# Kernel optimization log

Hardware: AMD Instinct MI355X
Metric: run time of the kernel (lower is better)

Reference implementation:

```python
import jax, jax.numpy as jnp
import numpy as np

N, E = 50000, 800000
IN_DIM, HIDDEN, HEADS, EDGE_DIM, OUT_DIM = 128, 64, 4, 16, 1
NEG_SLOPE = 0.2


def gat_conv(x, src, dst, edge_attr, W, We, att_src, att_dst, att_edge, bias, heads, out_ch, concat):
    n = x.shape[0]
    h = (x @ W).reshape(n, heads, out_ch)                     # [N,H,C]
    a_src = jnp.einsum('nhc,hc->nh', h, att_src)              # [N,H]
    a_dst = jnp.einsum('nhc,hc->nh', h, att_dst)
    e = (edge_attr @ We).reshape(-1, heads, out_ch)           # [E,H,C]
    a_e = jnp.einsum('ehc,hc->eh', e, att_edge)               # [E,H]
    alpha = jax.nn.leaky_relu(a_src[src] + a_dst[dst] + a_e, NEG_SLOPE)  # [E,H]
    # per-destination-node softmax
    amax = jax.ops.segment_max(alpha, dst, num_segments=n)
    ex = jnp.exp(alpha - amax[dst])
    denom = jax.ops.segment_sum(ex, dst, num_segments=n)
    alpha = ex / (denom[dst] + 1e-16)
    msg = h[src] * alpha[..., None]                           # [E,H,C]
    out = jax.ops.segment_sum(msg, dst, num_segments=n)       # [N,H,C]
    out = out.reshape(n, heads * out_ch) if concat else out.mean(axis=1)
    return out + bias


def setup_inputs() -> dict:
    key = jax.random.key(0)
    ks = jax.random.split(key, 16)
    s = 0.1
    inp = {
        'x': jax.random.normal(ks[0], (N, IN_DIM), jnp.float32),
        'edge_index': jax.random.randint(ks[1], (2, E), 0, N, jnp.int32),
        'edge_attr': jax.random.normal(ks[2], (E, EDGE_DIM), jnp.float32),
        # layer 1: heads=4, concat=True
        'W1': jax.random.normal(ks[3], (IN_DIM, HEADS * HIDDEN), jnp.float32) * s,
        'We1': jax.random.normal(ks[4], (EDGE_DIM, HEADS * HIDDEN), jnp.float32) * s,
        'as1': jax.random.normal(ks[5], (HEADS, HIDDEN), jnp.float32) * s,
        'ad1': jax.random.normal(ks[6], (HEADS, HIDDEN), jnp.float32) * s,
        'ae1': jax.random.normal(ks[7], (HEADS, HIDDEN), jnp.float32) * s,
        'b1': jnp.zeros((HEADS * HIDDEN,), jnp.float32),
        # layer 2: heads=1, concat=False
        'W2': jax.random.normal(ks[8], (HEADS * HIDDEN, HIDDEN), jnp.float32) * s,
        'We2': jax.random.normal(ks[9], (EDGE_DIM, HIDDEN), jnp.float32) * s,
        'as2': jax.random.normal(ks[10], (1, HIDDEN), jnp.float32) * s,
        'ad2': jax.random.normal(ks[11], (1, HIDDEN), jnp.float32) * s,
        'ae2': jax.random.normal(ks[12], (1, HIDDEN), jnp.float32) * s,
        'b2': jnp.zeros((HIDDEN,), jnp.float32),
        'Wlin': jax.random.normal(ks[13], (HIDDEN, OUT_DIM), jnp.float32) * s,
        'blin': jnp.zeros((OUT_DIM,), jnp.float32),
    }
    return inp


def reference(x, edge_index, edge_attr, W1, We1, as1, ad1, ae1, b1, W2, We2, as2, ad2, ae2, b2, Wlin, blin):
    src, dst = edge_index[0], edge_index[1]
    h = jax.nn.relu(gat_conv(x, src, dst, edge_attr, W1, We1, as1, ad1, ae1, b1, HEADS, HIDDEN, True))
    h = jax.nn.relu(gat_conv(h, src, dst, edge_attr, W2, We2, as2, ad2, ae2, b2, 1, HIDDEN, False))
    return h @ Wlin + blin
```

## Files before the change

### kernel.cpp

```cpp
#include <hip/hip_runtime.h>
#include <math.h>

#define IN_DIM 128
#define HID 64
#define HEADS 4
#define EDGE_DIM 16
#define L1_OUT 256
#define NEG_SLOPE 0.2f
#define PAD 64

typedef __attribute__((ext_vector_type(8))) _Float16 half8_t;
typedef __attribute__((ext_vector_type(4))) _Float16 half4_t;
typedef __attribute__((ext_vector_type(4))) float floatx4;

__global__ __launch_bounds__(256) void prep_kernel(
    const float* __restrict__ W1, const float* __restrict__ as1, const float* __restrict__ ad1,
    const float* __restrict__ W2, const float* __restrict__ as2, const float* __restrict__ ad2,
    const float* __restrict__ We1, const float* __restrict__ ae1,
    const float* __restrict__ We2, const float* __restrict__ ae2,
    _Float16* __restrict__ W1t, _Float16* __restrict__ W2t,
    float* __restrict__ q1, float* __restrict__ q2) {
    int id = blockIdx.x * 256 + threadIdx.x;
    if (id < 272 * 128) {
        int n = id >> 7, k = id & 127;
        float v = 0.f;
        if (n < 256) v = W1[k * 256 + n];
        else if (n < 260) { int h = n - 256; float s = 0.f;
            for (int c = 0; c < 64; ++c) s += W1[k * 256 + h * 64 + c] * as1[h * 64 + c]; v = s; }
        else if (n < 264) { int h = n - 260; float s = 0.f;
            for (int c = 0; c < 64; ++c) s += W1[k * 256 + h * 64 + c] * ad1[h * 64 + c]; v = s; }
        W1t[id] = (_Float16)v;
        return;
    }
    id -= 272 * 128;
    if (id < 80 * 256) {
        int n = id >> 8, k = id & 255;
        float v = 0.f;
        if (n < 64) v = W2[k * 64 + n];
        else if (n == 64) { float s = 0.f; for (int c = 0; c < 64; ++c) s += W2[k * 64 + c] * as2[c]; v = s; }
        else if (n == 65) { float s = 0.f; for (int c = 0; c < 64; ++c) s += W2[k * 64 + c] * ad2[c]; v = s; }
        W2t[id] = (_Float16)v;
        return;
    }
    id -= 80 * 256;
    if (id < 64) {
        int k = id >> 2, h = id & 3;
        float s = 0.f;
        for (int c = 0; c < 64; ++c) s += We1[k * 256 + h * 64 + c] * ae1[h * 64 + c];
        q1[id] = s;
        return;
    }
    id -= 64;
    if (id < 16) {
        float s = 0.f;
        for (int c = 0; c < 64; ++c) s += We2[id * 64 + c] * ae2[c];
        q2[id] = s;
    }
}

__global__ __launch_bounds__(256) void scatter_edge_kernel(
    const int* __restrict__ src, const int* __restrict__ dst,
    const float* __restrict__ ea, const float* __restrict__ q1,
    const float* __restrict__ q2, int* __restrict__ deg,
    float4* __restrict__ rec, int E) {
    __shared__ float q[80];
    if (threadIdx.x < 64) q[threadIdx.x] = q1[threadIdx.x];
    else if (threadIdx.x < 80) q[threadIdx.x] = q2[threadIdx.x - 64];
    __syncthreads();
    int e = blockIdx.x * 256 + threadIdx.x;
    if (e >= E) return;
    const float4* p = (const float4*)(ea + (size_t)e * EDGE_DIM);
    float4 v0 = p[0], v1 = p[1], v2 = p[2], v3 = p[3];
    int sn = src[e];
    int d = dst[e];
    float a[16] = {v0.x, v0.y, v0.z, v0.w, v1.x, v1.y, v1.z, v1.w,
                   v2.x, v2.y, v2.z, v2.w, v3.x, v3.y, v3.z, v3.w};
    float4 r1;
    float* rp = (float*)&r1;
#pragma unroll
    for (int h = 0; h < 4; ++h) {
        float s = 0.f;
#pragma unroll
        for (int k = 0; k < 16; ++k) s += a[k] * q[k * 4 + h];
        rp[h] = s;
    }
    float r2 = 0.f;
#pragma unroll
    for (int k = 0; k < 16; ++k) r2 += a[k] * q[64 + k];
    int rank = atomicAdd(&deg[d], 1);
    if (rank >= PAD) return;
    size_t pos = (size_t)d * PAD + rank;
    float4 lo;
    lo.x = __int_as_float(sn); lo.y = r2; lo.z = 0.f; lo.w = 0.f;
    rec[pos * 2] = lo;
    rec[pos * 2 + 1] = r1;
}

template <int NTOT, int NFEAT, int HATT, bool A32>
__global__ __launch_bounds__(256) void gemm_att_kernel(
    const void* __restrict__ Av, const _Float16* __restrict__ Bt,
    _Float16* __restrict__ C, float* __restrict__ asrc, float* __restrict__ adst,
    int M, int K) {
    __shared__ _Float16 As[64][72];
    __shared__ _Float16 Bts[NTOT * 16][72];
    const int tid = threadIdx.x;
    const int lane = tid & 63;
    const int w = tid >> 6;
    const int row0 = blockIdx.x * 64;
    const int m = lane & 15;
    const int quad = lane >> 4;

    floatx4 acc[NTOT];
#pragma unroll
    for (int t = 0; t < NTOT; ++t) acc[t] = (floatx4){0.f, 0.f, 0.f, 0.f};

    const int ar = tid >> 2;
    const int ac = (tid & 3) * 16;

    for (int k0 = 0; k0 < K; k0 += 64) {
        half8_t a0 = {}, a1 = {};
        if (row0 + ar < M) {
            if constexpr (A32) {
                const float* A = (const float*)Av + (size_t)(row0 + ar) * K + k0 + ac;
                const float4* f = (const float4*)A;
                float4 f0 = f[0], f1 = f[1], f2 = f[2], f3 = f[3];
                a0 = (half8_t){(_Float16)f0.x, (_Float16)f0.y, (_Float16)f0.z, (_Float16)f0.w,
                               (_Float16)f1.x, (_Float16)f1.y, (_Float16)f1.z, (_Float16)f1.w};
                a1 = (half8_t){(_Float16)f2.x, (_Float16)f2.y, (_Float16)f2.z, (_Float16)f2.w,
                               (_Float16)f3.x, (_Float16)f3.y, (_Float16)f3.z, (_Float16)f3.w};
            } else {
                const half8_t* g = (const half8_t*)((const _Float16*)Av + (size_t)(row0 + ar) * K + k0 + ac);
                a0 = g[0]; a1 = g[1];
            }
        }
        *(half8_t*)&As[ar][ac] = a0;
        *(half8_t*)&As[ar][ac + 8] = a1;
        for (int idx = tid; idx < NTOT * 128; idx += 256) {
            int n = idx >> 3, j = (idx & 7) * 8;
            *(half8_t*)&Bts[n][j] = *(const half8_t*)(Bt + (size_t)n * K + k0 + j);
        }
        __syncthreads();
#pragma unroll
        for (int kc = 0; kc < 2; ++kc) {
            half8_t af = *(const half8_t*)&As[w * 16 + m][kc * 32 + quad * 8];
#pragma unroll
            for (int t = 0; t < NTOT; ++t) {
                half8_t bf = *(const half8_t*)&Bts[t * 16 + m][kc * 32 + quad * 8];
                acc[t] = __builtin_amdgcn_mfma_f32_16x16x32_f16(af, bf, acc[t], 0, 0, 0);
            }
        }
        __syncthreads();
    }
    const int TE = NFEAT / 16;
#pragma unroll
    for (int r = 0; r < 4; ++r) {
        int row = row0 + w * 16 + quad * 4 + r;
        if (row >= M) continue;
#pragma unroll
        for (int t = 0; t < TE; ++t)
            C[(size_t)row * NFEAT + t * 16 + m] = (_Float16)acc[t][r];
        float v = acc[TE][r];
        if (m < HATT) asrc[row * HATT + m] = v;
        else if (m < 2 * HATT) adst[row * HATT + (m - HATT)] = v;
    }
}

__global__ __launch_bounds__(256) void node1_kernel(
    const int* __restrict__ deg, const float4* __restrict__ rec,
    const float* __restrict__ asrc1, const float* __restrict__ adst1,
    const _Float16* __restrict__ h1, const float* __restrict__ b1,
    _Float16* __restrict__ hr1, int Nn) {
    int lane = threadIdx.x & 63, wv = threadIdx.x >> 6;
    int n = blockIdx.x * 4 + wv;
    if (n >= Nn) return;
    int dg = __builtin_amdgcn_readfirstlane(deg[n]);
    if (dg > PAD) dg = PAD;
    size_t s0 = (size_t)n * PAD, s1 = s0 + dg;
    const int hh = lane >> 4;
    float adn = adst1[n * 4 + hh];
    const int* reci = (const int*)rec;
    const float* recf = (const float*)rec;

    float ax = 0.f, ay = 0.f, az = 0.f, aw = 0.f, l = 0.f;
    size_t s = s0;
    for (; s + 3 < s1; s += 4) {
        int i0 = reci[(s) * 8];
        int i1 = reci[(s + 1) * 8];
        int i2 = reci[(s + 2) * 8];
        int i3 = reci[(s + 3) * 8];
        float q0 = recf[(s) * 8 + 4 + hh];
        float q1v = recf[(s + 1) * 8 + 4 + hh];
        float q2v = recf[(s + 2) * 8 + 4 + hh];
        float q3 = recf[(s + 3) * 8 + 4 + hh];
        half4_t v0 = *(const half4_t*)(h1 + (size_t)i0 * L1_OUT + lane * 4);
        half4_t v1 = *(const half4_t*)(h1 + (size_t)i1 * L1_OUT + lane * 4);
        half4_t v2 = *(const half4_t*)(h1 + (size_t)i2 * L1_OUT + lane * 4);
        half4_t v3 = *(const half4_t*)(h1 + (size_t)i3 * L1_OUT + lane * 4);
        float t0 = q0 + asrc1[i0 * 4 + hh] + adn;
        float t1 = q1v + asrc1[i1 * 4 + hh] + adn;
        float t2 = q2v + asrc1[i2 * 4 + hh] + adn;
        float t3 = q3 + asrc1[i3 * 4 + hh] + adn;
        float e0 = __expf(t0 > 0.f ? t0 : NEG_SLOPE * t0);
        float e1 = __expf(t1 > 0.f ? t1 : NEG_SLOPE * t1);
        float e2 = __expf(t2 > 0.f ? t2 : NEG_SLOPE * t2);
        float e3 = __expf(t3 > 0.f ? t3 : NEG_SLOPE * t3);
        l += (e0 + e1) + (e2 + e3);
        ax += e0 * (float)v0.x + e1 * (float)v1.x + e2 * (float)v2.x + e3 * (float)v3.x;
        ay += e0 * (float)v0.y + e1 * (float)v1.y + e2 * (float)v2.y + e3 * (float)v3.y;
        az += e0 * (float)v0.z + e1 * (float)v1.z + e2 * (float)v2.z + e3 * (float)v3.z;
        aw += e0 * (float)v0.w + e1 * (float)v1.w + e2 * (float)v2.w + e3 * (float)v3.w;
    }
    for (; s < s1; ++s) {
        int i0 = reci[s * 8];
        float q0 = recf[s * 8 + 4 + hh];
        float t0 = q0 + asrc1[i0 * 4 + hh] + adn;
        half4_t v0 = *(const half4_t*)(h1 + (size_t)i0 * L1_OUT + lane * 4);
        float e0 = __expf(t0 > 0.f ? t0 : NEG_SLOPE * t0);
        l += e0;
        ax += e0 * (float)v0.x; ay += e0 * (float)v0.y;
        az += e0 * (float)v0.z; aw += e0 * (float)v0.w;
    }
    float inv = 1.f / (l + 1e-16f);
    float4 bb = *(const float4*)(b1 + lane * 4);
    half4_t out;
    out.x = (_Float16)fmaxf(ax * inv + bb.x, 0.f);
    out.y = (_Float16)fmaxf(ay * inv + bb.y, 0.f);
    out.z = (_Float16)fmaxf(az * inv + bb.z, 0.f);
    out.w = (_Float16)fmaxf(aw * inv + bb.w, 0.f);
    *(half4_t*)(hr1 + (size_t)n * L1_OUT + lane * 4) = out;
}

__global__ __launch_bounds__(256) void node2_kernel(
    const int* __restrict__ deg, const float4* __restrict__ rec,
    const float* __restrict__ asrc2, const float* __restrict__ adst2,
    const _Float16* __restrict__ h2, const float* __restrict__ b2,
    const float* __restrict__ Wlin, const float* __restrict__ blin,
    float* __restrict__ out, int Nn) {
    int lane = threadIdx.x & 63, wv = threadIdx.x >> 6;
    int n = blockIdx.x * 4 + wv;
    if (n >= Nn) return;
    int dg = __builtin_amdgcn_readfirstlane(deg[n]);
    if (dg > PAD) dg = PAD;
    size_t s0 = (size_t)n * PAD, s1 = s0 + dg;
    float adn = adst2[n];
    const int* reci = (const int*)rec;
    const float* recf = (const float*)rec;

    float l = 0.f, acc = 0.f;
    size_t s = s0;
    for (; s + 3 < s1; s += 4) {
        int n0 = reci[(s) * 8],     n1 = reci[(s + 1) * 8];
        int n2 = reci[(s + 2) * 8], n3 = reci[(s + 3) * 8];
        float q0 = recf[(s) * 8 + 1],     q1v = recf[(s + 1) * 8 + 1];
        float q2v = recf[(s + 2) * 8 + 1], q3 = recf[(s + 3) * 8 + 1];
        float t0 = q0 + asrc2[n0] + adn;
        float t1 = q1v + asrc2[n1] + adn;
        float t2 = q2v + asrc2[n2] + adn;
        float t3 = q3 + asrc2[n3] + adn;
        float v0 = (float)h2[(size_t)n0 * HID + lane];
        float v1 = (float)h2[(size_t)n1 * HID + lane];
        float v2 = (float)h2[(size_t)n2 * HID + lane];
        float v3 = (float)h2[(size_t)n3 * HID + lane];
        float e0 = __expf(t0 > 0.f ? t0 : NEG_SLOPE * t0);
        float e1 = __expf(t1 > 0.f ? t1 : NEG_SLOPE * t1);
        float e2 = __expf(t2 > 0.f ? t2 : NEG_SLOPE * t2);
        float e3 = __expf(t3 > 0.f ? t3 : NEG_SLOPE * t3);
        l += (e0 + e1) + (e2 + e3);
        acc += e0 * v0 + e1 * v1 + e2 * v2 + e3 * v3;
    }
    for (; s < s1; ++s) {
        int n0 = reci[s * 8];
        float q0 = recf[s * 8 + 1];
        float t0 = q0 + asrc2[n0] + adn;
        float e0 = __expf(t0 > 0.f ? t0 : NEG_SLOPE * t0);
        float v0 = (float)h2[(size_t)n0 * HID + lane];
        l += e0;
        acc += e0 * v0;
    }
    float res = fmaxf(acc / (l + 1e-16f) + b2[lane], 0.f);
    float t = res * Wlin[lane];
    for (int o = 32; o > 0; o >>= 1) t += __shfl_down(t, o);
    if (lane == 0) out[n] = t + blin[0];
}

extern "C" void kernel_launch(void* const* d_in, const int* in_sizes, int n_in,
                              void* d_out, int out_size, void* d_ws, size_t ws_size,
                              hipStream_t stream) {
    const float* x    = (const float*)d_in[0];
    const int*   ei   = (const int*)d_in[1];
    const float* ea   = (const float*)d_in[2];
    const float* W1   = (const float*)d_in[3];
    const float* We1  = (const float*)d_in[4];
    const float* as1  = (const float*)d_in[5];
    const float* ad1  = (const float*)d_in[6];
    const float* ae1  = (const float*)d_in[7];
    const float* b1   = (const float*)d_in[8];
    const float* W2   = (const float*)d_in[9];
    const float* We2  = (const float*)d_in[10];
    const float* as2  = (const float*)d_in[11];
    const float* ad2  = (const float*)d_in[12];
    const float* ae2  = (const float*)d_in[13];
    const float* b2   = (const float*)d_in[14];
    const float* Wlin = (const float*)d_in[15];
    const float* blin = (const float*)d_in[16];

    const int N = in_sizes[0] / IN_DIM;
    const int E = in_sizes[1] / 2;
    const int* src = ei;
    const int* dst = ei + E;

    char* base = (char*)d_ws;
    size_t off = 0;
    auto alloc = [&](size_t bytes) -> char* {
        char* p = base + off;
        off = (off + bytes + 255) & ~(size_t)255;
        return p;
    };
    int*      deg     = (int*)alloc((size_t)N * 4);
    float*    q1      = (float*)alloc(64 * 4);
    float*    q2      = (float*)alloc(16 * 4);
    _Float16* W1t     = (_Float16*)alloc((size_t)272 * 128 * 2);
    _Float16* W2t     = (_Float16*)alloc((size_t)80 * 256 * 2);
    float4*   rec     = (float4*)alloc((size_t)N * PAD * 32);
    float*    asrc1   = (float*)alloc((size_t)N * 4 * 4);
    float*    adst1   = (float*)alloc((size_t)N * 4 * 4);
    _Float16* h1      = (_Float16*)alloc((size_t)N * L1_OUT * 2);
    _Float16* hr1     = (_Float16*)alloc((size_t)N * L1_OUT * 2);
    _Float16* h2      = (_Float16*)alloc((size_t)N * HID * 2);
    float*    asrc2   = (float*)alloc((size_t)N * 4);
    float*    adst2   = (float*)alloc((size_t)N * 4);
    (void)ws_size; (void)n_in; (void)out_size;

    hipMemsetAsync(deg, 0, (size_t)N * 4, stream);
    prep_kernel<<<218, 256, 0, stream>>>(W1, as1, ad1, W2, as2, ad2,
                                         We1, ae1, We2, ae2, W1t, W2t, q1, q2);
    scatter_edge_kernel<<<(E + 255) / 256, 256, 0, stream>>>(src, dst, ea, q1, q2, deg,
                                                             rec, E);

    int mbl = (N + 63) / 64;
    gemm_att_kernel<17, 256, 4, true><<<mbl, 256, 0, stream>>>(x, W1t, h1, asrc1, adst1,
                                                               N, IN_DIM);
    node1_kernel<<<(N + 3) / 4, 256, 0, stream>>>(deg, rec, asrc1, adst1, h1, b1, hr1, N);
    gemm_att_kernel<5, 64, 1, false><<<mbl, 256, 0, stream>>>(hr1, W2t, h2, asrc2, adst2,
                                                              N, L1_OUT);
    node2_kernel<<<(N + 3) / 4, 256, 0, stream>>>(deg, rec, asrc2, adst2, h2, b2,
                                                  Wlin, blin, (float*)d_out, N);
}
```

Measured before the change: 326.2 us.

## Drop LDS staging in GEMMs and batch edge gathers 16-wide in node kernels

The GEMM kernel now loads A fragments and B fragments straight from global memory into registers with a compile-time K, removing the shared-memory staging and barriers. The node aggregation kernels now process 16 edges per step: each lane loads one edge record and computes its attention weight in parallel, then broadcasts source indices and weights through shuffles while issuing 16 independent feature gathers. This targets the serialized index-then-feature load latency chain in the gather loops. In exchange it adds more register pressure and redundant B loads from global/L2 per wave.

```diff
diff --git a/kernel.cpp b/kernel.cpp
--- a/kernel.cpp
+++ b/kernel.cpp
@@ -96,72 +96,68 @@
     rec[pos * 2 + 1] = r1;
 }
 
-template <int NTOT, int NFEAT, int HATT, bool A32>
+template <int NTOT, int NFEAT, int HATT, int KD, bool A32>
 __global__ __launch_bounds__(256) void gemm_att_kernel(
     const void* __restrict__ Av, const _Float16* __restrict__ Bt,
     _Float16* __restrict__ C, float* __restrict__ asrc, float* __restrict__ adst,
-    int M, int K) {
-    __shared__ _Float16 As[64][72];
-    __shared__ _Float16 Bts[NTOT * 16][72];
+    int M) {
+    constexpr int KC = KD / 32;
     const int tid = threadIdx.x;
     const int lane = tid & 63;
     const int w = tid >> 6;
-    const int row0 = blockIdx.x * 64;
     const int m = lane & 15;
     const int quad = lane >> 4;
+    const int row0 = blockIdx.x * 64;
+    const int arow = row0 + w * 16 + m;
+    const bool rv = arow < M;
+
+    half8_t af[KC];
+    if constexpr (A32) {
+        const float* A = (const float*)Av + (size_t)arow * KD + quad * 8;
+#pragma unroll
+        for (int kc = 0; kc < KC; ++kc) {
+            float4 f0 = {}, f1 = {};
+            if (rv) {
+                f0 = *(const float4*)(A + kc * 32);
+                f1 = *(const float4*)(A + kc * 32 + 4);
+            }
+            af[kc] = (half8_t){(_Float16)f0.x, (_Float16)f0.y, (_Float16)f0.z, (_Float16)f0.w,
+                               (_Float16)f1.x, (_Float16)f1.y, (_Float16)f1.z, (_Float16)f1.w};
+        }
+    } else {
+        const _Float16* A = (const _Float16*)Av + (size_t)arow * KD + quad * 8;
+#pragma unroll
+        for (int kc = 0; kc < KC; ++kc) {
+            half8_t a = {};
+            if (rv) a = *(const half8_t*)(A + kc * 32);
+            af[kc] = a;
+        }
+    }
 
     floatx4 acc[NTOT];
 #pragma unroll
     for (int t = 0; t < NTOT; ++t) acc[t] = (floatx4){0.f, 0.f, 0.f, 0.f};
-
-    const int ar = tid >> 2;
-    const int ac = (tid & 3) * 16;
-
-    for (int k0 = 0; k0 < K; k0 += 64) {
-        half8_t a0 = {}, a1 = {};
-        if (row0 + ar < M) {
-            if constexpr (A32) {
-                const float* A = (const float*)Av + (size_t)(row0 + ar) * K + k0 + ac;
-                const float4* f = (const float4*)A;
-                float4 f0 = f[0], f1 = f[1], f2 = f[2], f3 = f[3];
-                a0 = (half8_t){(_Float16)f0.x, (_Float16)f0.y, (_Float16)f0.z, (_Float16)f0.w,
-                               (_Float16)f1.x, (_Float16)f1.y, (_Float16)f1.z, (_Float16)f1.w};
-                a1 = (half8_t){(_Float16)f2.x, (_Float16)f2.y, (_Float16)f2.z, (_Float16)f2.w,
-                               (_Float16)f3.x, (_Float16)f3.y, (_Float16)f3.z, (_Float16)f3.w};
-            } else {
-                const half8_t* g = (const half8_t*)((const _Float16*)Av + (size_t)(row0 + ar) * K + k0 + ac);
-                a0 = g[0]; a1 = g[1];
-            }
-        }
-        *(half8_t*)&As[ar][ac] = a0;
-        *(half8_t*)&As[ar][ac + 8] = a1;
-        for (int idx = tid; idx < NTOT * 128; idx += 256) {
-            int n = idx >> 3, j = (idx & 7) * 8;
-            *(half8_t*)&Bts[n][j] = *(const half8_t*)(Bt + (size_t)n * K + k0 + j);
-        }
-        __syncthreads();
-#pragma unroll
-        for (int kc = 0; kc < 2; ++kc) {
-            half8_t af = *(const half8_t*)&As[w * 16 + m][kc * 32 + quad * 8];
-#pragma unroll
-            for (int t = 0; t < NTOT; ++t) {
-                half8_t bf = *(const half8_t*)&Bts[t * 16 + m][kc * 32 + quad * 8];
-                acc[t] = __builtin_amdgcn_mfma_f32_16x16x32_f16(af, bf, acc[t], 0, 0, 0);
-            }
-        }
-        __syncthreads();
-    }
+    const _Float16* Bp = Bt + (size_t)m * KD + quad * 8;
+#pragma unroll
+    for (int kc = 0; kc < KC; ++kc) {
+#pragma unroll
+        for (int t = 0; t < NTOT; ++t) {
+            half8_t bf = *(const half8_t*)(Bp + (size_t)t * 16 * KD + kc * 32);
+            acc[t] = __builtin_amdgcn_mfma_f32_16x16x32_f16(af[kc], bf, acc[t], 0, 0, 0);
+        }
+    }
+
     const int TE = NFEAT / 16;
 #pragma unroll
     for (int r = 0; r < 4; ++r) {
-        int row = row0 + w * 16 + quad * 4 + r;
-        if (row >= M) continue;
+        int orow = row0 + w * 16 + quad * 4 + r;
+        if (orow >= M) continue;
 #pragma unroll
         for (int t = 0; t < TE; ++t)
-            C[(size_t)row * NFEAT + t * 16 + m] = (_Float16)acc[t][r];
+            C[(size_t)orow * NFEAT + t * 16 + m] = (_Float16)acc[t][r];
         float v = acc[TE][r];
-        if (m < HATT) asrc[row * HATT + m] = v;
-        else if (m < 2 * HATT) adst[row * HATT + (m - HATT)] = v;
+        if (m < HATT) asrc[orow * HATT + m] = v;
+        else if (m < 2 * HATT) adst[orow * HATT + (m - HATT)] = v;
     }
 }
 
@@ -175,52 +171,42 @@
     if (n >= Nn) return;
     int dg = __builtin_amdgcn_readfirstlane(deg[n]);
     if (dg > PAD) dg = PAD;
-    size_t s0 = (size_t)n * PAD, s1 = s0 + dg;
+    const int j16 = lane & 15;
     const int hh = lane >> 4;
+    const int ebase = lane & 48;
     float adn = adst1[n * 4 + hh];
     const int* reci = (const int*)rec;
     const float* recf = (const float*)rec;
-
-    float ax = 0.f, ay = 0.f, az = 0.f, aw = 0.f, l = 0.f;
-    size_t s = s0;
-    for (; s + 3 < s1; s += 4) {
-        int i0 = reci[(s) * 8];
-        int i1 = reci[(s + 1) * 8];
-        int i2 = reci[(s + 2) * 8];
-        int i3 = reci[(s + 3) * 8];
-        float q0 = recf[(s) * 8 + 4 + hh];
-        float q1v = recf[(s + 1) * 8 + 4 + hh];
-        float q2v = recf[(s + 2) * 8 + 4 + hh];
-        float q3 = recf[(s + 3) * 8 + 4 + hh];
-        half4_t v0 = *(const half4_t*)(h1 + (size_t)i0 * L1_OUT + lane * 4);
-        half4_t v1 = *(const half4_t*)(h1 + (size_t)i1 * L1_OUT + lane * 4);
-        half4_t v2 = *(const half4_t*)(h1 + (size_t)i2 * L1_OUT + lane * 4);
-        half4_t v3 = *(const half4_t*)(h1 + (size_t)i3 * L1_OUT + lane * 4);
-        float t0 = q0 + asrc1[i0 * 4 + hh] + adn;
-        float t1 = q1v + asrc1[i1 * 4 + hh] + adn;
-        float t2 = q2v + asrc1[i2 * 4 + hh] + adn;
-        float t3 = q3 + asrc1[i3 * 4 + hh] + adn;
-        float e0 = __expf(t0 > 0.f ? t0 : NEG_SLOPE * t0);
-        float e1 = __expf(t1 > 0.f ? t1 : NEG_SLOPE * t1);
-        float e2 = __expf(t2 > 0.f ? t2 : NEG_SLOPE * t2);
-        float e3 = __expf(t3 > 0.f ? t3 : NEG_SLOPE * t3);
-        l += (e0 + e1) + (e2 + e3);
-        ax += e0 * (float)v0.x + e1 * (float)v1.x + e2 * (float)v2.x + e3 * (float)v3.x;
-        ay += e0 * (float)v0.y + e1 * (float)v1.y + e2 * (float)v2.y + e3 * (float)v3.y;
-        az += e0 * (float)v0.z + e1 * (float)v1.z + e2 * (float)v2.z + e3 * (float)v3.z;
-        aw += e0 * (float)v0.w + e1 * (float)v1.w + e2 * (float)v2.w + e3 * (float)v3.w;
-    }
-    for (; s < s1; ++s) {
-        int i0 = reci[s * 8];
-        float q0 = recf[s * 8 + 4 + hh];
-        float t0 = q0 + asrc1[i0 * 4 + hh] + adn;
-        half4_t v0 = *(const half4_t*)(h1 + (size_t)i0 * L1_OUT + lane * 4);
-        float e0 = __expf(t0 > 0.f ? t0 : NEG_SLOPE * t0);
-        l += e0;
-        ax += e0 * (float)v0.x; ay += e0 * (float)v0.y;
-        az += e0 * (float)v0.z; aw += e0 * (float)v0.w;
-    }
-    float inv = 1.f / (l + 1e-16f);
+    size_t s0 = (size_t)n * PAD;
+
+    float ax = 0.f, ay = 0.f, az = 0.f, aw = 0.f, lsum = 0.f;
+    for (int c0 = 0; c0 < dg; c0 += 16) {
+        int rem = dg - c0; if (rem > 16) rem = 16;
+        size_t srec = s0 + c0 + (j16 < rem ? j16 : 0);
+        int si = reci[srec * 8];
+        float qv = recf[srec * 8 + 4 + hh];
+        float av = asrc1[si * 4 + hh];
+        half4_t v[16];
+#pragma unroll
+        for (int j = 0; j < 16; ++j) {
+            int idx = __shfl(si, j);
+            v[j] = *(const half4_t*)(h1 + (size_t)idx * L1_OUT + lane * 4);
+        }
+        float t = qv + av + adn;
+        float e = (j16 < rem) ? __expf(t > 0.f ? t : NEG_SLOPE * t) : 0.f;
+        lsum += e;
+#pragma unroll
+        for (int j = 0; j < 16; ++j) {
+            float ej = __shfl(e, ebase | j);
+            ax += ej * (float)v[j].x;
+            ay += ej * (float)v[j].y;
+            az += ej * (float)v[j].z;
+            aw += ej * (float)v[j].w;
+        }
+    }
+#pragma unroll
+    for (int o = 1; o < 16; o <<= 1) lsum += __shfl_xor(lsum, o);
+    float inv = 1.f / (lsum + 1e-16f);
     float4 bb = *(const float4*)(b1 + lane * 4);
     half4_t out;
     out.x = (_Float16)fmaxf(ax * inv + bb.x, 0.f);
@@ -241,46 +227,40 @@
     if (n >= Nn) return;
     int dg = __builtin_amdgcn_readfirstlane(deg[n]);
     if (dg > PAD) dg = PAD;
-    size_t s0 = (size_t)n * PAD, s1 = s0 + dg;
+    const int j16 = lane & 15;
+    size_t s0 = (size_t)n * PAD;
     float adn = adst2[n];
     const int* reci = (const int*)rec;
     const float* recf = (const float*)rec;
 
-    float l = 0.f, acc = 0.f;
-    size_t s = s0;
-    for (; s + 3 < s1; s += 4) {
-        int n0 = reci[(s) * 8],     n1 = reci[(s + 1) * 8];
-        int n2 = reci[(s + 2) * 8], n3 = reci[(s + 3) * 8];
-        float q0 = recf[(s) * 8 + 1],     q1v = recf[(s + 1) * 8 + 1];
-        float q2v = recf[(s + 2) * 8 + 1], q3 = recf[(s + 3) * 8 + 1];
-        float t0 = q0 + asrc2[n0] + adn;
-        float t1 = q1v + asrc2[n1] + adn;
-        float t2 = q2v + asrc2[n2] + adn;
-        float t3 = q3 + asrc2[n3] + adn;
-        float v0 = (float)h2[(size_t)n0 * HID + lane];
-        float v1 = (float)h2[(size_t)n1 * HID + lane];
-        float v2 = (float)h2[(size_t)n2 * HID + lane];
-        float v3 = (float)h2[(size_t)n3 * HID + lane];
-        float e0 = __expf(t0 > 0.f ? t0 : NEG_SLOPE * t0);
-        float e1 = __expf(t1 > 0.f ? t1 : NEG_SLOPE * t1);
-        float e2 = __expf(t2 > 0.f ? t2 : NEG_SLOPE * t2);
-        float e3 = __expf(t3 > 0.f ? t3 : NEG_SLOPE * t3);
-        l += (e0 + e1) + (e2 + e3);
-        acc += e0 * v0 + e1 * v1 + e2 * v2 + e3 * v3;
-    }
-    for (; s < s1; ++s) {
-        int n0 = reci[s * 8];
-        float q0 = recf[s * 8 + 1];
-        float t0 = q0 + asrc2[n0] + adn;
-        float e0 = __expf(t0 > 0.f ? t0 : NEG_SLOPE * t0);
-        float v0 = (float)h2[(size_t)n0 * HID + lane];
-        l += e0;
-        acc += e0 * v0;
-    }
-    float res = fmaxf(acc / (l + 1e-16f) + b2[lane], 0.f);
-    float t = res * Wlin[lane];
-    for (int o = 32; o > 0; o >>= 1) t += __shfl_down(t, o);
-    if (lane == 0) out[n] = t + blin[0];
+    float lsum = 0.f, acc = 0.f;
+    for (int c0 = 0; c0 < dg; c0 += 16) {
+        int rem = dg - c0; if (rem > 16) rem = 16;
+        size_t srec = s0 + c0 + (j16 < rem ? j16 : 0);
+        int si = reci[srec * 8];
+        float qv = recf[srec * 8 + 1];
+        float av = asrc2[si];
+        _Float16 v[16];
+#pragma unroll
+        for (int j = 0; j < 16; ++j) {
+            int idx = __shfl(si, j);
+            v[j] = h2[(size_t)idx * HID + lane];
+        }
+        float t = qv + av + adn;
+        float e = (j16 < rem) ? __expf(t > 0.f ? t : NEG_SLOPE * t) : 0.f;
+        lsum += e;
+#pragma unroll
+        for (int j = 0; j < 16; ++j) {
+            float ej = __shfl(e, j);
+            acc += ej * (float)v[j];
+        }
+    }
+#pragma unroll
+    for (int o = 1; o < 16; o <<= 1) lsum += __shfl_xor(lsum, o);
+    float res = fmaxf(acc / (lsum + 1e-16f) + b2[lane], 0.f);
+    float t2 = res * Wlin[lane];
+    for (int o = 32; o > 0; o >>= 1) t2 += __shfl_down(t2, o);
+    if (lane == 0) out[n] = t2 + blin[0];
 }
 
 extern "C" void kernel_launch(void* const* d_in, const int* in_sizes, int n_in,
@@ -338,11 +318,11 @@
                                                              rec, E);
 
     int mbl = (N + 63) / 64;
-    gemm_att_kernel<17, 256, 4, true><<<mbl, 256, 0, stream>>>(x, W1t, h1, asrc1, adst1,
-                                                               N, IN_DIM);
+    gemm_att_kernel<17, 256, 4, 128, true><<<mbl, 256, 0, stream>>>(x, W1t, h1, asrc1,
+                                                                    adst1, N);
     node1_kernel<<<(N + 3) / 4, 256, 0, stream>>>(deg, rec, asrc1, adst1, h1, b1, hr1, N);
-    gemm_att_kernel<5, 64, 1, false><<<mbl, 256, 0, stream>>>(hr1, W2t, h2, asrc2, adst2,
-                                                              N, L1_OUT);
+    gemm_att_kernel<5, 64, 1, 256, false><<<mbl, 256, 0, stream>>>(hr1, W2t, h2, asrc2,
+                                                                   adst2, N);
     node2_kernel<<<(N + 3) / 4, 256, 0, stream>>>(deg, rec, asrc2, adst2, h2, b2,
                                                   Wlin, blin, (float*)d_out, N);
 }
```

Result: slower. 346.7 us (+6.3%).
